# Kernel tuning notes

Measured on AMD Instinct MI355X. Metric: run time of the kernel, lower is better.

## Reference

```python
import jax, jax.numpy as jnp
import numpy as np

N_NODES = 100000
N_EDGES = 1250000
IN_FEATS = 64
OUT_FEATS = 64


def setup_inputs() -> dict:
    key = jax.random.key(0)
    k_h, k_src, k_dst, k_w, k_b = jax.random.split(key, 5)
    h = jax.random.normal(k_h, (N_NODES, IN_FEATS), dtype=jnp.float32)
    src = jax.random.randint(k_src, (N_EDGES,), 0, N_NODES, dtype=jnp.int64)
    dst = jax.random.randint(k_dst, (N_EDGES,), 0, N_NODES, dtype=jnp.int64)
    # torch nn.Linear: weight [out, in], bias [out], uniform(-stdv, stdv)
    stdv = 1.0 / np.sqrt(IN_FEATS)
    W = jax.random.uniform(k_w, (OUT_FEATS, IN_FEATS), dtype=jnp.float32, minval=-stdv, maxval=stdv)
    b = jax.random.uniform(k_b, (OUT_FEATS,), dtype=jnp.float32, minval=-stdv, maxval=stdv)
    return {"h": h, "src": src, "dst": dst, "W": W, "b": b}


def reference(h, src, dst, W, b):
    # update_all(copy_src, sum): ah[v] = sum over edges (u->v) of h[u]
    msgs = h[src]                                   # [E, in] irregular gather
    ah = jax.ops.segment_sum(msgs, dst, num_segments=N_NODES)  # [N, in] scatter-add
    out = ah @ W.T + b                              # linear
    return jax.nn.relu(out)
```

## Files before the change

kernel.cpp:

```cpp
#include <hip/hip_runtime.h>

#define N_NODES 100000
#define N_EDGES 1250000
#define FEATS 64

#define NPB   128
#define NBUCK ((N_NODES + NPB - 1) / NPB)
#define CAP   2304
#define TILE  4096
#define NTILES ((N_EDGES + TILE - 1) / TILE)

typedef unsigned short ushort8 __attribute__((ext_vector_type(8)));

__device__ __forceinline__ float bf2f(unsigned short u) {
    return __uint_as_float(((unsigned int)u) << 16);
}
__device__ __forceinline__ unsigned short f2bf(float f) {
    unsigned int x = __float_as_uint(f);
    unsigned int lsb = (x >> 16) & 1u;
    x += 0x7fffu + lsb;
    return (unsigned short)(x >> 16);
}


__global__ __launch_bounds__(256) void binA_pack_kernel(
        const float* __restrict__ h,
        unsigned short* __restrict__ hb,
        const int* __restrict__ src,
        const int* __restrict__ dst,
        int* __restrict__ cursor,
        int* __restrict__ pairs) {
    const int PTOT = N_NODES * FEATS;
    for (int i = (blockIdx.x * 256 + threadIdx.x) * 8; i < PTOT;
         i += gridDim.x * 256 * 8) {
        float4 a = *(const float4*)(h + i);
        float4 c = *(const float4*)(h + i + 4);
        ushort8 u;
        u[0] = f2bf(a.x); u[1] = f2bf(a.y); u[2] = f2bf(a.z); u[3] = f2bf(a.w);
        u[4] = f2bf(c.x); u[5] = f2bf(c.y); u[6] = f2bf(c.z); u[7] = f2bf(c.w);
        *(ushort8*)(hb + i) = u;
    }

    __shared__ int hist[NBUCK];
    __shared__ int base[NBUCK];
    const int t  = threadIdx.x;
    const int e0 = blockIdx.x * TILE + t * 16;
    const bool full = (blockIdx.x + 1) * TILE <= N_EDGES;

    for (int i = t; i < NBUCK; i += 256) hist[i] = 0;
    __syncthreads();

    int d[16], lr[16];
    if (full) {
#pragma unroll
        for (int q = 0; q < 4; ++q) {
            int4 v = *(const int4*)(dst + e0 + q * 4);
            d[q * 4 + 0] = v.x; d[q * 4 + 1] = v.y;
            d[q * 4 + 2] = v.z; d[q * 4 + 3] = v.w;
        }
#pragma unroll
        for (int j = 0; j < 16; ++j) lr[j] = atomicAdd(&hist[d[j] >> 7], 1);
    } else {
#pragma unroll
        for (int j = 0; j < 16; ++j) {
            if (e0 + j < N_EDGES) {
                d[j]  = dst[e0 + j];
                lr[j] = atomicAdd(&hist[d[j] >> 7], 1);
            }
        }
    }
    __syncthreads();

    for (int i = t; i < NBUCK; i += 256)
        base[i] = hist[i] ? atomicAdd(&cursor[i], hist[i]) : 0;
    __syncthreads();

    if (full) {
        int s[16];
#pragma unroll
        for (int q = 0; q < 4; ++q) {
            int4 v = *(const int4*)(src + e0 + q * 4);
            s[q * 4 + 0] = v.x; s[q * 4 + 1] = v.y;
            s[q * 4 + 2] = v.z; s[q * 4 + 3] = v.w;
        }
#pragma unroll
        for (int j = 0; j < 16; ++j) {
            int bk  = d[j] >> 7;
            int rel = base[bk] + lr[j];
            if (rel < CAP)
                pairs[(size_t)bk * CAP + rel] = (s[j] << 7) | (d[j] & (NPB - 1));
        }
    } else {
#pragma unroll
        for (int j = 0; j < 16; ++j) {
            if (e0 + j < N_EDGES) {
                int bk  = d[j] >> 7;
                int rel = base[bk] + lr[j];
                if (rel < CAP)
                    pairs[(size_t)bk * CAP + rel] =
                        (src[e0 + j] << 7) | (d[j] & (NPB - 1));
            }
        }
    }
}

__global__ __launch_bounds__(256) void agg_kernel(
        const unsigned short* __restrict__ hb,
        const int* __restrict__ pairs,
        const int* __restrict__ cursor,
        const float* __restrict__ W,
        const float* __restrict__ bias,
        float* __restrict__ out) {
    __shared__ int   ssrc[CAP];
    __shared__ int   lcnt[NPB];
    __shared__ int   loff[NPB + 1];
    __shared__ int   lcur[NPB];
    __shared__ float srow[4][8][FEATS];

    const int tid  = threadIdx.x;
    const int lane = tid & 63;
    const int wv   = tid >> 6;
    const int g    = lane >> 3;
    const int li   = lane & 7;
    const int fo   = li * 8;

    float wr[FEATS];
#pragma unroll
    for (int kk = 0; kk < 16; ++kk) {
        float4 w4 = *(const float4*)(W + (size_t)lane * FEATS + kk * 4);
        wr[kk * 4 + 0] = w4.x;
        wr[kk * 4 + 1] = w4.y;
        wr[kk * 4 + 2] = w4.z;
        wr[kk * 4 + 3] = w4.w;
    }
    const float bv = bias[lane];

    const int b = blockIdx.x;
    int size = cursor[b];
    if (size > CAP) size = CAP;
    const int* bp = pairs + (size_t)b * CAP;

    if (tid < NPB) lcnt[tid] = 0;
    __syncthreads();
    for (int i = tid; i < size; i += 256) atomicAdd(&lcnt[bp[i] & (NPB - 1)], 1);
    __syncthreads();
    if (tid < NPB) lcur[tid] = lcnt[tid];
    __syncthreads();
    for (int off = 1; off < NPB; off <<= 1) {
        int y = 0;
        if (tid < NPB && tid >= off) y = lcur[tid - off];
        __syncthreads();
        if (tid < NPB) lcur[tid] += y;
        __syncthreads();
    }
    if (tid < NPB) loff[tid + 1] = lcur[tid];
    if (tid == 0) loff[0] = 0;
    __syncthreads();
    if (tid < NPB) lcur[tid] = loff[tid];
    __syncthreads();
    for (int i = tid; i < size; i += 256) {
        int p = bp[i];
        int r = atomicAdd(&lcur[p & (NPB - 1)], 1);
        ssrc[r] = p >> 7;
    }
    __syncthreads();

#pragma unroll
    for (int pass = 0; pass < 4; ++pass) {
        const int ln  = pass * 32 + wv * 8 + g;
        const int beg = loff[ln];
        const int m   = loff[ln + 1] - beg;

        float acc0[8], acc1[8];
#pragma unroll
        for (int i = 0; i < 8; ++i) { acc0[i] = 0.f; acc1[i] = 0.f; }

        for (int base = 0; __any(base < m); base += 8) {
#pragma unroll
            for (int t = 0; t < 8; t += 2) {
                const int i0 = base + t, i1 = base + t + 1;
                int r0 = (i0 < m) ? ssrc[beg + i0] : 0;
                int r1 = (i1 < m) ? ssrc[beg + i1] : 0;
                if (i0 < m) {
                    ushort8 u = *(const ushort8*)(hb + (size_t)r0 * FEATS + fo);
#pragma unroll
                    for (int i = 0; i < 8; ++i) acc0[i] += bf2f(u[i]);
                }
                if (i1 < m) {
                    ushort8 u = *(const ushort8*)(hb + (size_t)r1 * FEATS + fo);
#pragma unroll
                    for (int i = 0; i < 8; ++i) acc1[i] += bf2f(u[i]);
                }
            }
        }
#pragma unroll
        for (int i = 0; i < 8; ++i) acc0[i] += acc1[i];

        *(float4*)&srow[wv][g][fo]     = make_float4(acc0[0], acc0[1], acc0[2], acc0[3]);
        *(float4*)&srow[wv][g][fo + 4] = make_float4(acc0[4], acc0[5], acc0[6], acc0[7]);

        const int n0 = b * NPB + pass * 32 + wv * 8;
#pragma unroll
        for (int gg = 0; gg < 8; ++gg) {
            const int nn = n0 + gg;
            if (nn >= N_NODES) break;
            const float4* ar = (const float4*)&srow[wv][gg][0];
            float o_acc = bv;
#pragma unroll
            for (int k4 = 0; k4 < 16; ++k4) {
                float4 r = ar[k4];
                o_acc = fmaf(r.x, wr[k4 * 4 + 0], o_acc);
                o_acc = fmaf(r.y, wr[k4 * 4 + 1], o_acc);
                o_acc = fmaf(r.z, wr[k4 * 4 + 2], o_acc);
                o_acc = fmaf(r.w, wr[k4 * 4 + 3], o_acc);
            }
            out[(size_t)nn * FEATS + lane] = fmaxf(o_acc, 0.0f);
        }
    }
}

extern "C" void kernel_launch(void* const* d_in, const int* in_sizes, int n_in,
                              void* d_out, int out_size, void* d_ws, size_t ws_size,
                              hipStream_t stream) {
    const float* h   = (const float*)d_in[0];
    const int*   src = (const int*)d_in[1];
    const int*   dst = (const int*)d_in[2];
    const float* W   = (const float*)d_in[3];
    const float* b   = (const float*)d_in[4];
    float* out = (float*)d_out;

    int* cursor = (int*)d_ws;
    int* pairs  = cursor + 1024;
    unsigned short* hb = (unsigned short*)(pairs + (size_t)NBUCK * CAP);

    hipMemsetAsync(cursor, 0, 1024 * sizeof(int), stream);
    binA_pack_kernel<<<NTILES, 256, 0, stream>>>(h, hb, src, dst, cursor, pairs);
    agg_kernel<<<NBUCK, 256, 0, stream>>>(hb, pairs, cursor, W, b, out);
}
```

Baseline: 157.3 us.

## Apply linear transform before aggregation to drop per-node matmul in agg kernel

Uses linearity, sum(h[u])W^T = sum(h[u]W^T), to compute h·W^T once per node in the binning kernel and store it as bf16. The aggregation kernel then gathers transformed rows and only adds bias and applies ReLU, removing the shared-memory staging and the 64-FMA-per-output matvec from the gather kernel. The cost is a per-node matvec in the first kernel done with per-lane row reads and scalar 2-byte stores, which may be less coalesced than the old vectorized conversion. Rounding also changes, since the transformed values are rounded to bf16 before the sum instead of the raw features.

```diff
diff --git a/kernel.cpp b/kernel.cpp
--- a/kernel.cpp
+++ b/kernel.cpp
@@ -23,27 +23,50 @@
 }
 
 
-__global__ __launch_bounds__(256) void binA_pack_kernel(
+__global__ __launch_bounds__(256) void binA_wh_kernel(
         const float* __restrict__ h,
-        unsigned short* __restrict__ hb,
+        const float* __restrict__ W,
+        unsigned short* __restrict__ whb,
         const int* __restrict__ src,
         const int* __restrict__ dst,
         int* __restrict__ cursor,
         int* __restrict__ pairs) {
-    const int PTOT = N_NODES * FEATS;
-    for (int i = (blockIdx.x * 256 + threadIdx.x) * 8; i < PTOT;
-         i += gridDim.x * 256 * 8) {
-        float4 a = *(const float4*)(h + i);
-        float4 c = *(const float4*)(h + i + 4);
-        ushort8 u;
-        u[0] = f2bf(a.x); u[1] = f2bf(a.y); u[2] = f2bf(a.z); u[3] = f2bf(a.w);
-        u[4] = f2bf(c.x); u[5] = f2bf(c.y); u[6] = f2bf(c.z); u[7] = f2bf(c.w);
-        *(ushort8*)(hb + i) = u;
+    const int t    = threadIdx.x;
+    const int lane = t & 63;
+    const int wv   = t >> 6;
+
+    {
+        float wr[FEATS];
+#pragma unroll
+        for (int kk = 0; kk < 16; ++kk) {
+            float4 w4 = *(const float4*)(W + (size_t)lane * FEATS + kk * 4);
+            wr[kk * 4 + 0] = w4.x;
+            wr[kk * 4 + 1] = w4.y;
+            wr[kk * 4 + 2] = w4.z;
+            wr[kk * 4 + 3] = w4.w;
+        }
+        const int NW    = NTILES * 4;
+        const int CHUNK = (N_NODES + NW - 1) / NW;
+        const int wid   = blockIdx.x * 4 + wv;
+        const int n0 = wid * CHUNK;
+        int n1 = n0 + CHUNK; if (n1 > N_NODES) n1 = N_NODES;
+        for (int n = n0; n < n1; ++n) {
+            const float* hr = h + (size_t)n * FEATS;
+            float acc = 0.f;
+#pragma unroll
+            for (int kk = 0; kk < 16; ++kk) {
+                float4 h4 = *(const float4*)(hr + kk * 4);
+                acc = fmaf(h4.x, wr[kk * 4 + 0], acc);
+                acc = fmaf(h4.y, wr[kk * 4 + 1], acc);
+                acc = fmaf(h4.z, wr[kk * 4 + 2], acc);
+                acc = fmaf(h4.w, wr[kk * 4 + 3], acc);
+            }
+            whb[(size_t)n * FEATS + lane] = f2bf(acc);
+        }
     }
 
     __shared__ int hist[NBUCK];
     __shared__ int base[NBUCK];
-    const int t  = threadIdx.x;
     const int e0 = blockIdx.x * TILE + t * 16;
     const bool full = (blockIdx.x + 1) * TILE <= N_EDGES;
 
@@ -105,17 +128,15 @@
 }
 
 __global__ __launch_bounds__(256) void agg_kernel(
-        const unsigned short* __restrict__ hb,
+        const unsigned short* __restrict__ whb,
         const int* __restrict__ pairs,
         const int* __restrict__ cursor,
-        const float* __restrict__ W,
         const float* __restrict__ bias,
         float* __restrict__ out) {
-    __shared__ int   ssrc[CAP];
-    __shared__ int   lcnt[NPB];
-    __shared__ int   loff[NPB + 1];
-    __shared__ int   lcur[NPB];
-    __shared__ float srow[4][8][FEATS];
+    __shared__ int ssrc[CAP];
+    __shared__ int lcnt[NPB];
+    __shared__ int loff[NPB + 1];
+    __shared__ int lcur[NPB];
 
     const int tid  = threadIdx.x;
     const int lane = tid & 63;
@@ -124,16 +145,8 @@
     const int li   = lane & 7;
     const int fo   = li * 8;
 
-    float wr[FEATS];
-#pragma unroll
-    for (int kk = 0; kk < 16; ++kk) {
-        float4 w4 = *(const float4*)(W + (size_t)lane * FEATS + kk * 4);
-        wr[kk * 4 + 0] = w4.x;
-        wr[kk * 4 + 1] = w4.y;
-        wr[kk * 4 + 2] = w4.z;
-        wr[kk * 4 + 3] = w4.w;
-    }
-    const float bv = bias[lane];
+    const float4 bv0 = *(const float4*)(bias + fo);
+    const float4 bv1 = *(const float4*)(bias + fo + 4);
 
     const int b = blockIdx.x;
     int size = cursor[b];
@@ -182,39 +195,31 @@
                 int r0 = (i0 < m) ? ssrc[beg + i0] : 0;
                 int r1 = (i1 < m) ? ssrc[beg + i1] : 0;
                 if (i0 < m) {
-                    ushort8 u = *(const ushort8*)(hb + (size_t)r0 * FEATS + fo);
+                    ushort8 u = *(const ushort8*)(whb + (size_t)r0 * FEATS + fo);
 #pragma unroll
                     for (int i = 0; i < 8; ++i) acc0[i] += bf2f(u[i]);
                 }
                 if (i1 < m) {
-                    ushort8 u = *(const ushort8*)(hb + (size_t)r1 * FEATS + fo);
+                    ushort8 u = *(const ushort8*)(whb + (size_t)r1 * FEATS + fo);
 #pragma unroll
                     for (int i = 0; i < 8; ++i) acc1[i] += bf2f(u[i]);
                 }
             }
         }
-#pragma unroll
-        for (int i = 0; i < 8; ++i) acc0[i] += acc1[i];
-
-        *(float4*)&srow[wv][g][fo]     = make_float4(acc0[0], acc0[1], acc0[2], acc0[3]);
-        *(float4*)&srow[wv][g][fo + 4] = make_float4(acc0[4], acc0[5], acc0[6], acc0[7]);
-
-        const int n0 = b * NPB + pass * 32 + wv * 8;
-#pragma unroll
-        for (int gg = 0; gg < 8; ++gg) {
-            const int nn = n0 + gg;
-            if (nn >= N_NODES) break;
-            const float4* ar = (const float4*)&srow[wv][gg][0];
-            float o_acc = bv;
-#pragma unroll
-            for (int k4 = 0; k4 < 16; ++k4) {
-                float4 r = ar[k4];
-                o_acc = fmaf(r.x, wr[k4 * 4 + 0], o_acc);
-                o_acc = fmaf(r.y, wr[k4 * 4 + 1], o_acc);
-                o_acc = fmaf(r.z, wr[k4 * 4 + 2], o_acc);
-                o_acc = fmaf(r.w, wr[k4 * 4 + 3], o_acc);
-            }
-            out[(size_t)nn * FEATS + lane] = fmaxf(o_acc, 0.0f);
+
+        const int nn = b * NPB + ln;
+        if (nn < N_NODES) {
+            float4 o0, o1;
+            o0.x = fmaxf(acc0[0] + acc1[0] + bv0.x, 0.f);
+            o0.y = fmaxf(acc0[1] + acc1[1] + bv0.y, 0.f);
+            o0.z = fmaxf(acc0[2] + acc1[2] + bv0.z, 0.f);
+            o0.w = fmaxf(acc0[3] + acc1[3] + bv0.w, 0.f);
+            o1.x = fmaxf(acc0[4] + acc1[4] + bv1.x, 0.f);
+            o1.y = fmaxf(acc0[5] + acc1[5] + bv1.y, 0.f);
+            o1.z = fmaxf(acc0[6] + acc1[6] + bv1.z, 0.f);
+            o1.w = fmaxf(acc0[7] + acc1[7] + bv1.w, 0.f);
+            *(float4*)(out + (size_t)nn * FEATS + fo)     = o0;
+            *(float4*)(out + (size_t)nn * FEATS + fo + 4) = o1;
         }
     }
 }
@@ -231,9 +236,9 @@
 
     int* cursor = (int*)d_ws;
     int* pairs  = cursor + 1024;
-    unsigned short* hb = (unsigned short*)(pairs + (size_t)NBUCK * CAP);
+    unsigned short* whb = (unsigned short*)(pairs + (size_t)NBUCK * CAP);
 
     hipMemsetAsync(cursor, 0, 1024 * sizeof(int), stream);
-    binA_pack_kernel<<<NTILES, 256, 0, stream>>>(h, hb, src, dst, cursor, pairs);
-    agg_kernel<<<NBUCK, 256, 0, stream>>>(hb, pairs, cursor, W, b, out);
-}
+    binA_wh_kernel<<<NTILES, 256, 0, stream>>>(h, W, whb, src, dst, cursor, pairs);
+    agg_kernel<<<NBUCK, 256, 0, stream>>>(whb, pairs, cursor, b, out);
+}
```

Result: slower. 229.1 us (+45.6%).
